# Optimization experiments

Hardware: AMD Instinct MI355X
Metric: run time of the kernel (lower is better)

The kernel has to match this reference:

```python
import jax, jax.numpy as jnp
import numpy as np

B, N, D, H = 4, 1024, 1024, 16
NP = N - 1  # prototypes; +1 CLS slot -> n_valid == N
HD = D // H
LN_EPS = 1e-5


def _build_spatial_sim(key):
    centers = jax.random.uniform(key, (NP, 2), dtype=jnp.float32) * 10.0
    diff = centers[:, None, :] - centers[None, :, :]
    d2 = jnp.sum(diff * diff, axis=-1)           # squared pairwise distance
    dist = jnp.sqrt(d2)
    sigma = dist.mean()                           # spatial_sigma = mean cdist
    sim = jnp.exp(-d2 / (2.0 * sigma * sigma))
    sim = sim / sim.max()
    ext = jnp.zeros((NP + 1, NP + 1), dtype=jnp.float32)
    ext = ext.at[0, :].set(1.0).at[:, 0].set(1.0).at[1:, 1:].set(sim)
    return ext


def setup_inputs() -> dict:
    key = jax.random.key(0)
    kc, kx, kq, kp = jax.random.split(key, 4)
    spatial_sim = _build_spatial_sim(kc)          # [N, N] buffer
    x = jax.random.normal(kx, (B, N, D), dtype=jnp.float32)
    gamma = jnp.ones((D,), dtype=jnp.float32)
    beta = jnp.zeros((D,), dtype=jnp.float32)
    w_qkv = jax.random.normal(kq, (D, 3 * D), dtype=jnp.float32) * 0.02
    w_proj = jax.random.normal(kp, (D, D), dtype=jnp.float32) * 0.02
    b_proj = jnp.zeros((D,), dtype=jnp.float32)
    swl = jnp.float32(np.log(0.3 / 0.7))          # inverse_sigmoid(0.3)
    return {"x": x, "gamma": gamma, "beta": beta, "w_qkv": w_qkv,
            "w_proj": w_proj, "b_proj": b_proj,
            "spatial_weight_logit": swl, "spatial_sim": spatial_sim}


def reference(x, gamma, beta, w_qkv, w_proj, b_proj, spatial_weight_logit, spatial_sim):
    b, n, d = x.shape
    scale = HD ** (-0.5)
    # LayerNorm (biased variance, eps=1e-5)
    mu = x.mean(axis=-1, keepdims=True)
    var = jnp.mean((x - mu) ** 2, axis=-1, keepdims=True)
    x_norm = (x - mu) / jnp.sqrt(var + LN_EPS) * gamma + beta
    # QKV projection -> [B, H, N, HD] each
    qkv = (x_norm @ w_qkv).reshape(b, n, 3, H, HD)
    qkv = jnp.transpose(qkv, (2, 0, 3, 1, 4))
    q, k, v = qkv[0], qkv[1], qkv[2]
    scores = jnp.einsum('bhnd,bhmd->bhnm', q, k) * scale
    alpha = jax.nn.sigmoid(spatial_weight_logit)
    # blend feature attention with fixed spatial similarity, then softmax
    attn = jax.nn.softmax((1.0 - alpha) * scores + alpha * spatial_sim[None, None], axis=-1)
    out = jnp.einsum('bhnm,bhmd->bhnd', attn, v)
    out = jnp.transpose(out, (0, 2, 1, 3)).reshape(b, n, d)
    out = out @ w_proj + b_proj
    return x + out
```

## Files before the change

kernel.cpp:

```cpp
#include <hip/hip_runtime.h>

#define Bz 4
#define Nn 1024
#define Dd 1024
#define Hh 16
#define HD 64
#define SCALE 0.125f
#define LN_EPS 1e-5f

typedef __attribute__((ext_vector_type(8))) __bf16 bf16x8;
typedef __attribute__((ext_vector_type(4))) float f32x4;

static __device__ inline unsigned short f2bf(float f) {
    unsigned int u = __float_as_uint(f);
    u += 0x7fffu + ((u >> 16) & 1u);
    return (unsigned short)(u >> 16);
}

static __device__ inline bf16x8 ldfrag(const unsigned short* p) {
    return *(const bf16x8*)p;
}

static __device__ __forceinline__ void glds16(const unsigned short* g, unsigned short* l) {
    __builtin_amdgcn_global_load_lds((const __attribute__((address_space(1))) void*)g,
                                     (__attribute__((address_space(3))) void*)l, 16, 0, 0);
}

__global__ __launch_bounds__(256) void prep_kernel(const float* __restrict__ x,
                                                   const float* __restrict__ gamma,
                                                   const float* __restrict__ beta,
                                                   unsigned short* __restrict__ xn,
                                                   const float* __restrict__ w_qkv,
                                                   unsigned short* __restrict__ wqkvT,
                                                   const float* __restrict__ w_proj,
                                                   unsigned short* __restrict__ wprojT) {
    __shared__ float tile[32][33];
    int blk = blockIdx.x;
    int tid = threadIdx.x;

    if (blk < 4096) {
        const float* xr = x + (size_t)blk * Dd;
        float4 v = ((const float4*)xr)[tid];
        float s = v.x + v.y + v.z + v.w;
        float ss = v.x * v.x + v.y * v.y + v.z * v.z + v.w * v.w;
        for (int o = 32; o > 0; o >>= 1) {
            s += __shfl_down(s, o);
            ss += __shfl_down(ss, o);
        }
        float* red = &tile[0][0];
        int wid = tid >> 6;
        if ((tid & 63) == 0) { red[wid * 2] = s; red[wid * 2 + 1] = ss; }
        __syncthreads();
        float tot = red[0] + red[2] + red[4] + red[6];
        float tot2 = red[1] + red[3] + red[5] + red[7];
        float mu = tot * (1.0f / Dd);
        float var = tot2 * (1.0f / Dd) - mu * mu;
        float inv = rsqrtf(var + LN_EPS);
        float4 g = ((const float4*)gamma)[tid];
        float4 b = ((const float4*)beta)[tid];
        ushort4 o4;
        o4.x = f2bf((v.x - mu) * inv * g.x + b.x);
        o4.y = f2bf((v.y - mu) * inv * g.y + b.y);
        o4.z = f2bf((v.z - mu) * inv * g.z + b.z);
        o4.w = f2bf((v.w - mu) * inv * g.w + b.w);
        ((ushort4*)(xn + (size_t)blk * Dd))[tid] = o4;
    } else {
        const float* in;
        unsigned short* out;
        int cols, c0, r0;
        if (blk < 7168) {
            int idx = blk - 4096;
            in = w_qkv; out = wqkvT; cols = 3072;
            c0 = (idx % 96) * 32; r0 = (idx / 96) * 32;
        } else {
            int idx = blk - 7168;
            in = w_proj; out = wprojT; cols = 1024;
            c0 = (idx % 32) * 32; r0 = (idx / 32) * 32;
        }
        int tx = tid & 31, ty = tid >> 5;
        #pragma unroll
        for (int i = 0; i < 32; i += 8)
            tile[ty + i][tx] = in[(size_t)(r0 + ty + i) * cols + c0 + tx];
        __syncthreads();
        #pragma unroll
        for (int i = 0; i < 32; i += 8)
            out[(size_t)(c0 + ty + i) * 1024 + r0 + tx] = f2bf(tile[tx][ty + i]);
    }
}


__global__ __launch_bounds__(256) void gemm_qkv(const unsigned short* __restrict__ A,
                                                const unsigned short* __restrict__ Bt,
                                                unsigned short* __restrict__ qb,
                                                unsigned short* __restrict__ kb,
                                                unsigned short* __restrict__ vtb) {
    __shared__ unsigned short sA[8192], sB[8192];
    int tid = threadIdx.x;
    int w = tid >> 6, lane = tid & 63, lrow = lane & 15, quad = lane >> 4;
    int wm = w >> 1, wn = w & 1;
    int rowbase = blockIdx.y * 128;
    int colbase = blockIdx.x * 128;

    int srow = tid >> 3;
    int gch = ((tid & 7) - (srow >> 1)) & 7;
    const unsigned short* gA = A + (size_t)(rowbase + srow) * 1024 + gch * 8;
    const unsigned short* gB = Bt + (size_t)(colbase + srow) * 1024 + gch * 8;
    unsigned short* lA = sA + w * 512;
    unsigned short* lB = sB + w * 512;

    int bs0 = ((quad + (lrow >> 1)) & 7) * 8;
    int bs1 = ((4 + quad + (lrow >> 1)) & 7) * 8;
    const unsigned short* fa = sA + (wm * 64 + lrow) * 64;
    const unsigned short* fb = sB + (wn * 64 + lrow) * 64;

    f32x4 acc[4][4];
    #pragma unroll
    for (int i = 0; i < 4; i++)
        #pragma unroll
        for (int j = 0; j < 4; j++)
            acc[i][j] = (f32x4){0.f, 0.f, 0.f, 0.f};

    for (int k0 = 0; k0 < 1024; k0 += 64) {
        __syncthreads();
        #pragma unroll
        for (int c = 0; c < 4; c++) {
            glds16(gA + (size_t)c * 32768 + k0, lA + c * 2048);
            glds16(gB + (size_t)c * 32768 + k0, lB + c * 2048);
        }
        __syncthreads();
        #pragma unroll
        for (int s = 0; s < 2; s++) {
            int bo = s ? bs1 : bs0;
            bf16x8 a[4], b[4];
            #pragma unroll
            for (int i = 0; i < 4; i++) a[i] = *(const bf16x8*)(fa + i * 1024 + bo);
            #pragma unroll
            for (int j = 0; j < 4; j++) b[j] = *(const bf16x8*)(fb + j * 1024 + bo);
            #pragma unroll
            for (int i = 0; i < 4; i++)
                #pragma unroll
                for (int j = 0; j < 4; j++)
                    acc[i][j] = __builtin_amdgcn_mfma_f32_16x16x32_bf16(a[i], b[j], acc[i][j], 0, 0, 0);
        }
    }

    if (colbase < 2048) {
        #pragma unroll
        for (int j = 0; j < 4; j++) {
            int col = colbase + wn * 64 + j * 16 + lrow;
            int s = col >> 10, rem = col & 1023;
            int h = rem >> 6, e = rem & 63;
            unsigned short* dst = (s == 0) ? qb : kb;
            #pragma unroll
            for (int i = 0; i < 4; i++) {
                #pragma unroll
                for (int r = 0; r < 4; r++) {
                    int R = rowbase + wm * 64 + i * 16 + quad * 4 + r;
                    int bb = R >> 10, n = R & 1023;
                    dst[(((size_t)(bb * Hh + h)) * Nn + n) * HD + e] = f2bf(acc[i][j][r]);
                }
            }
        }
    } else {
        int bb = rowbase >> 10;
        int nbase = (rowbase & 1023) + wm * 64;
        unsigned short* sc = sA + w * 2048;
        int er = lane >> 2, nc = lane & 3;
        #pragma unroll
        for (int j = 0; j < 4; j++) {
            __syncthreads();
            int ebase = colbase + wn * 64 + j * 16 - 2048;
            int h = ebase >> 6, e0 = ebase & 63;
            #pragma unroll
            for (int i = 0; i < 4; i++) {
                uint2 pk;
                pk.x = (unsigned)f2bf(acc[i][j][0]) | ((unsigned)f2bf(acc[i][j][1]) << 16);
                pk.y = (unsigned)f2bf(acc[i][j][2]) | ((unsigned)f2bf(acc[i][j][3]) << 16);
                *(uint2*)(sc + lrow * 68 + i * 16 + quad * 4) = pk;
            }
            __syncthreads();
            unsigned short* vrow = vtb + ((size_t)((bb * Hh + h) * HD) + e0 + er) * Nn + nbase;
            #pragma unroll
            for (int c = 0; c < 4; c++) {
                uint2 v = *(const uint2*)(sc + er * 68 + c * 16 + nc * 4);
                *(uint2*)(vrow + c * 16 + nc * 4) = v;
            }
        }
    }
}

__global__ __launch_bounds__(256) void gemm_proj(const unsigned short* __restrict__ A,
                                                 const unsigned short* __restrict__ Bt,
                                                 const float* __restrict__ bias,
                                                 const float* __restrict__ x,
                                                 float* __restrict__ out) {
    __shared__ unsigned short sA[8192], sB[8192];
    int tid = threadIdx.x;
    int w = tid >> 6, lane = tid & 63, lrow = lane & 15, quad = lane >> 4;
    int wm = w >> 1, wn = w & 1;
    int rowbase = blockIdx.y * 128;
    int colbase = blockIdx.x * 128;

    int srow = tid >> 3;
    int gch = ((tid & 7) - (srow >> 1)) & 7;
    const unsigned short* gA = A + (size_t)(rowbase + srow) * 1024 + gch * 8;
    const unsigned short* gB = Bt + (size_t)(colbase + srow) * 1024 + gch * 8;
    unsigned short* lA = sA + w * 512;
    unsigned short* lB = sB + w * 512;

    int bs0 = ((quad + (lrow >> 1)) & 7) * 8;
    int bs1 = ((4 + quad + (lrow >> 1)) & 7) * 8;
    const unsigned short* fa = sA + (wm * 64 + lrow) * 64;
    const unsigned short* fb = sB + (wn * 64 + lrow) * 64;

    f32x4 acc[4][4];
    #pragma unroll
    for (int i = 0; i < 4; i++)
        #pragma unroll
        for (int j = 0; j < 4; j++)
            acc[i][j] = (f32x4){0.f, 0.f, 0.f, 0.f};

    for (int k0 = 0; k0 < 1024; k0 += 64) {
        __syncthreads();
        #pragma unroll
        for (int c = 0; c < 4; c++) {
            glds16(gA + (size_t)c * 32768 + k0, lA + c * 2048);
            glds16(gB + (size_t)c * 32768 + k0, lB + c * 2048);
        }
        __syncthreads();
        #pragma unroll
        for (int s = 0; s < 2; s++) {
            int bo = s ? bs1 : bs0;
            bf16x8 a[4], b[4];
            #pragma unroll
            for (int i = 0; i < 4; i++) a[i] = *(const bf16x8*)(fa + i * 1024 + bo);
            #pragma unroll
            for (int j = 0; j < 4; j++) b[j] = *(const bf16x8*)(fb + j * 1024 + bo);
            #pragma unroll
            for (int i = 0; i < 4; i++)
                #pragma unroll
                for (int j = 0; j < 4; j++)
                    acc[i][j] = __builtin_amdgcn_mfma_f32_16x16x32_bf16(a[i], b[j], acc[i][j], 0, 0, 0);
        }
    }

    #pragma unroll
    for (int j = 0; j < 4; j++) {
        int col = colbase + wn * 64 + j * 16 + lrow;
        float bc = bias[col];
        #pragma unroll
        for (int i = 0; i < 4; i++) {
            #pragma unroll
            for (int r = 0; r < 4; r++) {
                int R = rowbase + wm * 64 + i * 16 + quad * 4 + r;
                out[(size_t)R * 1024 + col] = acc[i][j][r] + bc + x[(size_t)R * 1024 + col];
            }
        }
    }
}

#define PSTR 72
#define LOG2E 1.4426950408889634f
__global__ __launch_bounds__(256) void attn_kernel(const unsigned short* __restrict__ qb,
                                                   const unsigned short* __restrict__ kb,
                                                   const unsigned short* __restrict__ vtb,
                                                   const float* __restrict__ sim,
                                                   const float* __restrict__ swl,
                                                   unsigned short* __restrict__ aout) {
    int h = blockIdx.y, bb = blockIdx.z;
    int n0 = blockIdx.x * 128;
    int tid = threadIdx.x;
    int w = tid >> 6, lane = tid & 63;
    int lrow = lane & 15, quad = lane >> 4;
    const unsigned short* q = qb + ((size_t)(bb * Hh + h)) * Nn * HD;
    const unsigned short* k = kb + ((size_t)(bb * Hh + h)) * Nn * HD;
    const unsigned short* vt = vtb + ((size_t)(bb * Hh + h)) * HD * Nn;
    float alpha = 1.f / (1.f + __expf(-swl[0]));
    float c1 = (1.f - alpha) * SCALE * LOG2E;
    float a2 = alpha * LOG2E;

    __shared__ unsigned short sK[4096];
    __shared__ unsigned short sV[4096];
    __shared__ unsigned short sP[128 * PSTR];

    int qr0 = n0 + w * 32;
    bf16x8 qf[2][2];
    #pragma unroll
    for (int g = 0; g < 2; g++) {
        qf[g][0] = ldfrag(q + (size_t)(qr0 + g * 16 + lrow) * HD + quad * 8);
        qf[g][1] = ldfrag(q + (size_t)(qr0 + g * 16 + lrow) * HD + 32 + quad * 8);
    }

    f32x4 o[2][4];
    #pragma unroll
    for (int g = 0; g < 2; g++)
        #pragma unroll
        for (int et = 0; et < 4; et++) o[g][et] = (f32x4){0.f, 0.f, 0.f, 0.f};
    float rsum[2] = {0.f, 0.f};

    int bs0 = (quad + (lrow >> 1)) & 7;
    int bs1 = (4 + quad + (lrow >> 1)) & 7;
    unsigned short* sPw = sP + (w * 32) * PSTR;

    for (int m0 = 0; m0 < 1024; m0 += 64) {
        __syncthreads();
        #pragma unroll
        for (int i = 0; i < 2; i++) {
            int slot = i * 256 + tid;
            int row = slot >> 3;
            int cg = ((slot & 7) - (row >> 1)) & 7;
            glds16(k + (size_t)(m0 + row) * HD + cg * 8, sK + i * 2048 + w * 512);
        }
        #pragma unroll
        for (int i = 0; i < 2; i++) {
            int slot = i * 256 + tid;
            int row = slot >> 3;
            int cg = ((slot & 7) - (row >> 1)) & 7;
            glds16(vt + (size_t)row * Nn + m0 + cg * 8, sV + i * 2048 + w * 512);
        }
        float4 sm[4][2];
        #pragma unroll
        for (int ks = 0; ks < 4; ks++)
            #pragma unroll
            for (int g = 0; g < 2; g++)
                sm[ks][g] = *(const float4*)(sim + (size_t)(qr0 + g * 16 + lrow) * Nn
                                             + m0 + ks * 16 + quad * 4);
        __syncthreads();

        #pragma unroll
        for (int ks = 0; ks < 4; ks++) {
            const unsigned short* kr = sK + (ks * 16 + lrow) * 64;
            bf16x8 ak0 = *(const bf16x8*)(kr + bs0 * 8);
            bf16x8 ak1 = *(const bf16x8*)(kr + bs1 * 8);
            #pragma unroll
            for (int g = 0; g < 2; g++) {
                f32x4 c = (f32x4){0.f, 0.f, 0.f, 0.f};
                c = __builtin_amdgcn_mfma_f32_16x16x32_bf16(ak0, qf[g][0], c, 0, 0, 0);
                c = __builtin_amdgcn_mfma_f32_16x16x32_bf16(ak1, qf[g][1], c, 0, 0, 0);
                float e0 = __builtin_amdgcn_exp2f(c1 * c[0] + a2 * sm[ks][g].x);
                float e1 = __builtin_amdgcn_exp2f(c1 * c[1] + a2 * sm[ks][g].y);
                float e2 = __builtin_amdgcn_exp2f(c1 * c[2] + a2 * sm[ks][g].z);
                float e3 = __builtin_amdgcn_exp2f(c1 * c[3] + a2 * sm[ks][g].w);
                rsum[g] += (e0 + e1) + (e2 + e3);
                uint2 pk;
                pk.x = (__float_as_uint(e0) >> 16) | (__float_as_uint(e1) & 0xffff0000u);
                pk.y = (__float_as_uint(e2) >> 16) | (__float_as_uint(e3) & 0xffff0000u);
                *(uint2*)(sPw + (g * 16 + lrow) * PSTR + ks * 16 + quad * 4) = pk;
            }
        }

        __builtin_amdgcn_s_setprio(1);
        #pragma unroll
        for (int ms = 0; ms < 2; ms++) {
            bf16x8 pa[2];
            #pragma unroll
            for (int g = 0; g < 2; g++)
                pa[g] = *(const bf16x8*)(sPw + (g * 16 + lrow) * PSTR + ms * 32 + quad * 8);
            #pragma unroll
            for (int et = 0; et < 4; et++) {
                int e = et * 16 + lrow;
                int slot = (ms * 4 + quad + (e >> 1)) & 7;
                bf16x8 vb = *(const bf16x8*)(sV + e * 64 + slot * 8);
                #pragma unroll
                for (int g = 0; g < 2; g++)
                    o[g][et] = __builtin_amdgcn_mfma_f32_16x16x32_bf16(pa[g], vb, o[g][et], 0, 0, 0);
            }
        }
        __builtin_amdgcn_s_setprio(0);
    }

    #pragma unroll
    for (int g = 0; g < 2; g++) {
        rsum[g] += __shfl_xor(rsum[g], 16);
        rsum[g] += __shfl_xor(rsum[g], 32);
    }

    #pragma unroll
    for (int g = 0; g < 2; g++)
        #pragma unroll
        for (int r = 0; r < 4; r++) {
            float inv = 1.f / __shfl(rsum[g], quad * 4 + r);
            int qn = qr0 + g * 16 + quad * 4 + r;
            #pragma unroll
            for (int et = 0; et < 4; et++)
                aout[((size_t)bb * Nn + qn) * Dd + h * HD + et * 16 + lrow]
                    = f2bf(o[g][et][r] * inv);
        }
}

extern "C" void kernel_launch(void* const* d_in, const int* in_sizes, int n_in,
                              void* d_out, int out_size, void* d_ws, size_t ws_size,
                              hipStream_t stream) {
    const float* x      = (const float*)d_in[0];
    const float* gamma  = (const float*)d_in[1];
    const float* beta   = (const float*)d_in[2];
    const float* w_qkv  = (const float*)d_in[3];
    const float* w_proj = (const float*)d_in[4];
    const float* b_proj = (const float*)d_in[5];
    const float* swl    = (const float*)d_in[6];
    const float* sim    = (const float*)d_in[7];
    float* out = (float*)d_out;

    unsigned short* ws = (unsigned short*)d_ws;
    unsigned short* xn     = ws;
    unsigned short* wqkvT  = xn + 4194304;
    unsigned short* wprojT = wqkvT + 3145728;
    unsigned short* qb     = wprojT + 1048576;
    unsigned short* kb     = qb + 4194304;
    unsigned short* vtb    = kb + 4194304;
    unsigned short* aout   = vtb + 4194304;

    prep_kernel<<<8192, 256, 0, stream>>>(x, gamma, beta, xn, w_qkv, wqkvT, w_proj, wprojT);
    gemm_qkv<<<dim3(24, 32), 256, 0, stream>>>(xn, wqkvT, qb, kb, vtb);
    attn_kernel<<<dim3(8, 16, 4), 256, 0, stream>>>(qb, kb, vtb, sim, swl, aout);
    gemm_proj<<<dim3(8, 32), 256, 0, stream>>>(aout, wprojT, b_proj, x, out);
}
```

Baseline: 195.9 us.

## Double-buffer K/V tiles and use 8 waves of 16 query rows in attention

```diff
diff --git a/kernel.cpp b/kernel.cpp
--- a/kernel.cpp
+++ b/kernel.cpp
@@ -261,12 +261,12 @@
 
 #define PSTR 72
 #define LOG2E 1.4426950408889634f
-__global__ __launch_bounds__(256) void attn_kernel(const unsigned short* __restrict__ qb,
-                                                   const unsigned short* __restrict__ kb,
-                                                   const unsigned short* __restrict__ vtb,
-                                                   const float* __restrict__ sim,
-                                                   const float* __restrict__ swl,
-                                                   unsigned short* __restrict__ aout) {
+__global__ __launch_bounds__(512, 4) void attn_kernel(const unsigned short* __restrict__ qb,
+                                                      const unsigned short* __restrict__ kb,
+                                                      const unsigned short* __restrict__ vtb,
+                                                      const float* __restrict__ sim,
+                                                      const float* __restrict__ swl,
+                                                      unsigned short* __restrict__ aout) {
     int h = blockIdx.y, bb = blockIdx.z;
     int n0 = blockIdx.x * 128;
     int tid = threadIdx.x;
@@ -279,113 +279,106 @@
     float c1 = (1.f - alpha) * SCALE * LOG2E;
     float a2 = alpha * LOG2E;
 
-    __shared__ unsigned short sK[4096];
-    __shared__ unsigned short sV[4096];
+    __shared__ unsigned short sK[2][4096];
+    __shared__ unsigned short sV[2][4096];
     __shared__ unsigned short sP[128 * PSTR];
 
-    int qr0 = n0 + w * 32;
-    bf16x8 qf[2][2];
-    #pragma unroll
-    for (int g = 0; g < 2; g++) {
-        qf[g][0] = ldfrag(q + (size_t)(qr0 + g * 16 + lrow) * HD + quad * 8);
-        qf[g][1] = ldfrag(q + (size_t)(qr0 + g * 16 + lrow) * HD + 32 + quad * 8);
-    }
-
-    f32x4 o[2][4];
-    #pragma unroll
-    for (int g = 0; g < 2; g++)
-        #pragma unroll
-        for (int et = 0; et < 4; et++) o[g][et] = (f32x4){0.f, 0.f, 0.f, 0.f};
-    float rsum[2] = {0.f, 0.f};
+    int qr0 = n0 + w * 16;
+    bf16x8 qf0 = ldfrag(q + (size_t)(qr0 + lrow) * HD + quad * 8);
+    bf16x8 qf1 = ldfrag(q + (size_t)(qr0 + lrow) * HD + 32 + quad * 8);
+
+    f32x4 o[4];
+    #pragma unroll
+    for (int et = 0; et < 4; et++) o[et] = (f32x4){0.f, 0.f, 0.f, 0.f};
+    float rsum = 0.f;
 
     int bs0 = (quad + (lrow >> 1)) & 7;
     int bs1 = (4 + quad + (lrow >> 1)) & 7;
-    unsigned short* sPw = sP + (w * 32) * PSTR;
-
-    for (int m0 = 0; m0 < 1024; m0 += 64) {
-        __syncthreads();
-        #pragma unroll
-        for (int i = 0; i < 2; i++) {
-            int slot = i * 256 + tid;
-            int row = slot >> 3;
-            int cg = ((slot & 7) - (row >> 1)) & 7;
-            glds16(k + (size_t)(m0 + row) * HD + cg * 8, sK + i * 2048 + w * 512);
-        }
-        #pragma unroll
-        for (int i = 0; i < 2; i++) {
-            int slot = i * 256 + tid;
-            int row = slot >> 3;
-            int cg = ((slot & 7) - (row >> 1)) & 7;
-            glds16(vt + (size_t)row * Nn + m0 + cg * 8, sV + i * 2048 + w * 512);
-        }
-        float4 sm[4][2];
-        #pragma unroll
-        for (int ks = 0; ks < 4; ks++)
-            #pragma unroll
-            for (int g = 0; g < 2; g++)
-                sm[ks][g] = *(const float4*)(sim + (size_t)(qr0 + g * 16 + lrow) * Nn
-                                             + m0 + ks * 16 + quad * 4);
-        __syncthreads();
-
+    unsigned short* sPw = sP + (w * 16) * PSTR;
+
+    int srow = tid >> 3;
+    int cg = ((tid & 7) - (srow >> 1)) & 7;
+    const unsigned short* gK = k + (size_t)srow * HD + cg * 8;
+    const unsigned short* gV = vt + (size_t)srow * Nn + cg * 8;
+    const float* gS = sim + (size_t)(qr0 + lrow) * Nn + quad * 4;
+    unsigned short* lK0 = &sK[0][0] + w * 512;
+    unsigned short* lV0 = &sV[0][0] + w * 512;
+    unsigned short* lK1 = &sK[1][0] + w * 512;
+    unsigned short* lV1 = &sV[1][0] + w * 512;
+
+    glds16(gK, lK0);
+    glds16(gV, lV0);
+    float4 sm[4];
+    #pragma unroll
+    for (int ks = 0; ks < 4; ks++) sm[ks] = *(const float4*)(gS + ks * 16);
+    __syncthreads();
+
+    for (int t = 0; t < 16; t++) {
+        int cur = t & 1;
+        float4 smN[4];
+        if (t < 15) {
+            int m1 = (t + 1) * 64;
+            glds16(gK + (size_t)m1 * HD, cur ? lK0 : lK1);
+            glds16(gV + m1, cur ? lV0 : lV1);
+            #pragma unroll
+            for (int ks = 0; ks < 4; ks++)
+                smN[ks] = *(const float4*)(gS + m1 + ks * 16);
+        }
+
+        const unsigned short* sKc = sK[cur];
+        const unsigned short* sVc = sV[cur];
         #pragma unroll
         for (int ks = 0; ks < 4; ks++) {
-            const unsigned short* kr = sK + (ks * 16 + lrow) * 64;
+            const unsigned short* kr = sKc + (ks * 16 + lrow) * 64;
             bf16x8 ak0 = *(const bf16x8*)(kr + bs0 * 8);
             bf16x8 ak1 = *(const bf16x8*)(kr + bs1 * 8);
-            #pragma unroll
-            for (int g = 0; g < 2; g++) {
-                f32x4 c = (f32x4){0.f, 0.f, 0.f, 0.f};
-                c = __builtin_amdgcn_mfma_f32_16x16x32_bf16(ak0, qf[g][0], c, 0, 0, 0);
-                c = __builtin_amdgcn_mfma_f32_16x16x32_bf16(ak1, qf[g][1], c, 0, 0, 0);
-                float e0 = __builtin_amdgcn_exp2f(c1 * c[0] + a2 * sm[ks][g].x);
-                float e1 = __builtin_amdgcn_exp2f(c1 * c[1] + a2 * sm[ks][g].y);
-                float e2 = __builtin_amdgcn_exp2f(c1 * c[2] + a2 * sm[ks][g].z);
-                float e3 = __builtin_amdgcn_exp2f(c1 * c[3] + a2 * sm[ks][g].w);
-                rsum[g] += (e0 + e1) + (e2 + e3);
-                uint2 pk;
-                pk.x = (__float_as_uint(e0) >> 16) | (__float_as_uint(e1) & 0xffff0000u);
-                pk.y = (__float_as_uint(e2) >> 16) | (__float_as_uint(e3) & 0xffff0000u);
-                *(uint2*)(sPw + (g * 16 + lrow) * PSTR + ks * 16 + quad * 4) = pk;
-            }
+            f32x4 c = (f32x4){0.f, 0.f, 0.f, 0.f};
+            c = __builtin_amdgcn_mfma_f32_16x16x32_bf16(ak0, qf0, c, 0, 0, 0);
+            c = __builtin_amdgcn_mfma_f32_16x16x32_bf16(ak1, qf1, c, 0, 0, 0);
+            float e0 = __builtin_amdgcn_exp2f(c1 * c[0] + a2 * sm[ks].x);
+            float e1 = __builtin_amdgcn_exp2f(c1 * c[1] + a2 * sm[ks].y);
+            float e2 = __builtin_amdgcn_exp2f(c1 * c[2] + a2 * sm[ks].z);
+            float e3 = __builtin_amdgcn_exp2f(c1 * c[3] + a2 * sm[ks].w);
+            rsum += (e0 + e1) + (e2 + e3);
+            uint2 pk;
+            pk.x = (__float_as_uint(e0) >> 16) | (__float_as_uint(e1) & 0xffff0000u);
+            pk.y = (__float_as_uint(e2) >> 16) | (__float_as_uint(e3) & 0xffff0000u);
+            *(uint2*)(sPw + lrow * PSTR + ks * 16 + quad * 4) = pk;
         }
 
         __builtin_amdgcn_s_setprio(1);
         #pragma unroll
         for (int ms = 0; ms < 2; ms++) {
-            bf16x8 pa[2];
-            #pragma unroll
-            for (int g = 0; g < 2; g++)
-                pa[g] = *(const bf16x8*)(sPw + (g * 16 + lrow) * PSTR + ms * 32 + quad * 8);
+            bf16x8 pa = *(const bf16x8*)(sPw + lrow * PSTR + ms * 32 + quad * 8);
             #pragma unroll
             for (int et = 0; et < 4; et++) {
                 int e = et * 16 + lrow;
                 int slot = (ms * 4 + quad + (e >> 1)) & 7;
-                bf16x8 vb = *(const bf16x8*)(sV + e * 64 + slot * 8);
-                #pragma unroll
-                for (int g = 0; g < 2; g++)
-                    o[g][et] = __builtin_amdgcn_mfma_f32_16x16x32_bf16(pa[g], vb, o[g][et], 0, 0, 0);
+                bf16x8 vb = *(const bf16x8*)(sVc + e * 64 + slot * 8);
+                o[et] = __builtin_amdgcn_mfma_f32_16x16x32_bf16(pa, vb, o[et], 0, 0, 0);
             }
         }
         __builtin_amdgcn_s_setprio(0);
-    }
-
-    #pragma unroll
-    for (int g = 0; g < 2; g++) {
-        rsum[g] += __shfl_xor(rsum[g], 16);
-        rsum[g] += __shfl_xor(rsum[g], 32);
-    }
-
-    #pragma unroll
-    for (int g = 0; g < 2; g++)
-        #pragma unroll
-        for (int r = 0; r < 4; r++) {
-            float inv = 1.f / __shfl(rsum[g], quad * 4 + r);
-            int qn = qr0 + g * 16 + quad * 4 + r;
-            #pragma unroll
-            for (int et = 0; et < 4; et++)
-                aout[((size_t)bb * Nn + qn) * Dd + h * HD + et * 16 + lrow]
-                    = f2bf(o[g][et][r] * inv);
-        }
+
+        __syncthreads();
+        if (t < 15) {
+            #pragma unroll
+            for (int ks = 0; ks < 4; ks++) sm[ks] = smN[ks];
+        }
+    }
+
+    rsum += __shfl_xor(rsum, 16);
+    rsum += __shfl_xor(rsum, 32);
+
+    #pragma unroll
+    for (int r = 0; r < 4; r++) {
+        float inv = 1.f / __shfl(rsum, quad * 4 + r);
+        int qn = qr0 + quad * 4 + r;
+        #pragma unroll
+        for (int et = 0; et < 4; et++)
+            aout[((size_t)bb * Nn + qn) * Dd + h * HD + et * 16 + lrow]
+                = f2bf(o[et][r] * inv);
+    }
 }
 
 extern "C" void kernel_launch(void* const* d_in, const int* in_sizes, int n_in,
@@ -412,6 +405,6 @@
 
     prep_kernel<<<8192, 256, 0, stream>>>(x, gamma, beta, xn, w_qkv, wqkvT, w_proj, wprojT);
     gemm_qkv<<<dim3(24, 32), 256, 0, stream>>>(xn, wqkvT, qb, kb, vtb);
-    attn_kernel<<<dim3(8, 16, 4), 256, 0, stream>>>(qb, kb, vtb, sim, swl, aout);
+    attn_kernel<<<dim3(8, 16, 4), 512, 0, stream>>>(qb, kb, vtb, sim, swl, aout);
     gemm_proj<<<dim3(8, 32), 256, 0, stream>>>(aout, wprojT, b_proj, x, out);
 }
```

Result: no change. 194.5 us (-0.7%).

## Double-buffer K tiles and prefetch sim, load V fragments directly to registers

Applied to the files above, without the earlier changes.

```diff
diff --git a/kernel.cpp b/kernel.cpp
--- a/kernel.cpp
+++ b/kernel.cpp
@@ -261,12 +261,12 @@
 
 #define PSTR 72
 #define LOG2E 1.4426950408889634f
-__global__ __launch_bounds__(256) void attn_kernel(const unsigned short* __restrict__ qb,
-                                                   const unsigned short* __restrict__ kb,
-                                                   const unsigned short* __restrict__ vtb,
-                                                   const float* __restrict__ sim,
-                                                   const float* __restrict__ swl,
-                                                   unsigned short* __restrict__ aout) {
+__global__ __launch_bounds__(256, 2) void attn_kernel(const unsigned short* __restrict__ qb,
+                                                      const unsigned short* __restrict__ kb,
+                                                      const unsigned short* __restrict__ vtb,
+                                                      const float* __restrict__ sim,
+                                                      const float* __restrict__ swl,
+                                                      unsigned short* __restrict__ aout) {
     int h = blockIdx.y, bb = blockIdx.z;
     int n0 = blockIdx.x * 128;
     int tid = threadIdx.x;
@@ -279,8 +279,7 @@
     float c1 = (1.f - alpha) * SCALE * LOG2E;
     float a2 = alpha * LOG2E;
 
-    __shared__ unsigned short sK[4096];
-    __shared__ unsigned short sV[4096];
+    __shared__ unsigned short sK[2][4096];
     __shared__ unsigned short sP[128 * PSTR];
 
     int qr0 = n0 + w * 32;
@@ -302,34 +301,54 @@
     int bs1 = (4 + quad + (lrow >> 1)) & 7;
     unsigned short* sPw = sP + (w * 32) * PSTR;
 
-    for (int m0 = 0; m0 < 1024; m0 += 64) {
-        __syncthreads();
-        #pragma unroll
-        for (int i = 0; i < 2; i++) {
-            int slot = i * 256 + tid;
-            int row = slot >> 3;
-            int cg = ((slot & 7) - (row >> 1)) & 7;
-            glds16(k + (size_t)(m0 + row) * HD + cg * 8, sK + i * 2048 + w * 512);
-        }
-        #pragma unroll
-        for (int i = 0; i < 2; i++) {
-            int slot = i * 256 + tid;
-            int row = slot >> 3;
-            int cg = ((slot & 7) - (row >> 1)) & 7;
-            glds16(vt + (size_t)row * Nn + m0 + cg * 8, sV + i * 2048 + w * 512);
-        }
-        float4 sm[4][2];
-        #pragma unroll
-        for (int ks = 0; ks < 4; ks++)
-            #pragma unroll
-            for (int g = 0; g < 2; g++)
-                sm[ks][g] = *(const float4*)(sim + (size_t)(qr0 + g * 16 + lrow) * Nn
-                                             + m0 + ks * 16 + quad * 4);
-        __syncthreads();
-
+    int c0i = tid, c1i = 256 + tid;
+    int row0 = c0i >> 3, cg0 = ((c0i & 7) - (row0 >> 1)) & 7;
+    int row1 = c1i >> 3, cg1 = ((c1i & 7) - (row1 >> 1)) & 7;
+    const unsigned short* gK0 = k + (size_t)row0 * HD + cg0 * 8;
+    const unsigned short* gK1 = k + (size_t)row1 * HD + cg1 * 8;
+    const float* gS0 = sim + (size_t)(qr0 + lrow) * Nn + quad * 4;
+    const float* gS1 = gS0 + (size_t)16 * Nn;
+
+    glds16(gK0, &sK[0][0] + tid * 8);
+    glds16(gK1, &sK[0][0] + 2048 + tid * 8);
+    float4 sm[4][2];
+    #pragma unroll
+    for (int ks = 0; ks < 4; ks++) {
+        sm[ks][0] = *(const float4*)(gS0 + ks * 16);
+        sm[ks][1] = *(const float4*)(gS1 + ks * 16);
+    }
+    __syncthreads();
+
+    for (int t = 0; t < 16; t++) {
+        int cur = t & 1;
+        int m0 = t * 64;
+
+        bf16x8 vreg[2][4];
+        #pragma unroll
+        for (int ms = 0; ms < 2; ms++)
+            #pragma unroll
+            for (int et = 0; et < 4; et++) {
+                int e = et * 16 + lrow;
+                vreg[ms][et] = *(const bf16x8*)(vt + (size_t)e * Nn + m0 + ms * 32 + quad * 8);
+            }
+
+        float4 smN[4][2];
+        if (t < 15) {
+            int m1 = m0 + 64;
+            unsigned short* dst = &sK[cur ^ 1][0];
+            glds16(gK0 + (size_t)m1 * HD, dst + tid * 8);
+            glds16(gK1 + (size_t)m1 * HD, dst + 2048 + tid * 8);
+            #pragma unroll
+            for (int ks = 0; ks < 4; ks++) {
+                smN[ks][0] = *(const float4*)(gS0 + m1 + ks * 16);
+                smN[ks][1] = *(const float4*)(gS1 + m1 + ks * 16);
+            }
+        }
+
+        const unsigned short* sKc = sK[cur];
         #pragma unroll
         for (int ks = 0; ks < 4; ks++) {
-            const unsigned short* kr = sK + (ks * 16 + lrow) * 64;
+            const unsigned short* kr = sKc + (ks * 16 + lrow) * 64;
             bf16x8 ak0 = *(const bf16x8*)(kr + bs0 * 8);
             bf16x8 ak1 = *(const bf16x8*)(kr + bs1 * 8);
             #pragma unroll
@@ -357,16 +376,21 @@
             for (int g = 0; g < 2; g++)
                 pa[g] = *(const bf16x8*)(sPw + (g * 16 + lrow) * PSTR + ms * 32 + quad * 8);
             #pragma unroll
-            for (int et = 0; et < 4; et++) {
-                int e = et * 16 + lrow;
-                int slot = (ms * 4 + quad + (e >> 1)) & 7;
-                bf16x8 vb = *(const bf16x8*)(sV + e * 64 + slot * 8);
+            for (int et = 0; et < 4; et++)
                 #pragma unroll
                 for (int g = 0; g < 2; g++)
-                    o[g][et] = __builtin_amdgcn_mfma_f32_16x16x32_bf16(pa[g], vb, o[g][et], 0, 0, 0);
-            }
+                    o[g][et] = __builtin_amdgcn_mfma_f32_16x16x32_bf16(pa[g], vreg[ms][et], o[g][et], 0, 0, 0);
         }
         __builtin_amdgcn_s_setprio(0);
+
+        __syncthreads();
+        if (t < 15) {
+            #pragma unroll
+            for (int ks = 0; ks < 4; ks++) {
+                sm[ks][0] = smN[ks][0];
+                sm[ks][1] = smN[ks][1];
+            }
+        }
     }
 
     #pragma unroll
```

Result: slower. 215.5 us (+10.0%).
